# Kernel tuning notes

Measured on AMD Instinct MI355X. Metric: run time of the kernel, lower is better.

Reference implementation:

```python
import jax, jax.numpy as jnp
import numpy as np

ALPHA = 0.2  # LeakyReLU negative slope


def setup_inputs() -> dict:
    key = jax.random.key(0)
    k1, k2, k3, k4 = jax.random.split(key, 4)
    N, E, d_in, d_out = 100000, 1600000, 64, 64
    node_features = jax.random.normal(k1, (N, d_in), dtype=jnp.float32)
    edge_index = jax.random.randint(k2, (2, E), 0, N, dtype=jnp.int64)
    # learned params: W is Linear(in,out,bias=False) weight used as x @ W.T; store as [d_in,d_out]
    W = jax.random.normal(k3, (d_in, d_out), dtype=jnp.float32) * (1.414 * np.sqrt(2.0 / (d_in + d_out)))
    a = jax.random.normal(k4, (2 * d_out,), dtype=jnp.float32) * (1.414 * np.sqrt(2.0 / (2 * d_out + 1)))
    return {"node_features": node_features, "edge_index": edge_index, "W": W, "a": a}


def reference(node_features, edge_index, W, a):
    N = node_features.shape[0]
    d_out = W.shape[1]
    src, tgt = edge_index[0], edge_index[1]

    h = node_features @ W  # [N, d_out]
    # a([h_src, h_tgt]) == h_src @ a[:d] + h_tgt @ a[d:]; compute node-level scores once
    s_src = h @ a[:d_out]   # [N]
    s_tgt = h @ a[d_out:]   # [N]
    e = jax.nn.leaky_relu(s_src[src] + s_tgt[tgt], negative_slope=ALPHA)  # [E]

    # per-target segment softmax (stable): scatter-max, exp, scatter-sum
    m = jax.ops.segment_max(e, tgt, num_segments=N)          # [N]
    e_exp = jnp.exp(e - m[tgt])                              # [E]
    denom = jax.ops.segment_sum(e_exp, tgt, num_segments=N)  # [N]
    attention = e_exp / denom[tgt]                           # [E]
    # dropout is identity in eval mode (training=False)

    # weighted scatter-add of source features into targets
    h_prime = jax.ops.segment_sum(h[src] * attention[:, None], tgt, num_segments=N)  # [N, d_out]
    return jax.nn.elu(h_prime)
```

## Files before the change

kernel.cpp:

```cpp
#include <hip/hip_runtime.h>
#include <hip/hip_bf16.h>
#include <math.h>

#define ALPHA  0.2f
#define BSH    7
#define BNODES 128
#define NBMAX  1024
#define K_CH   4096
#define CAPB   3584

static __device__ __forceinline__ unsigned short f2bf(float x) {
    __hip_bfloat16 b = __float2bfloat16(x);
    return *reinterpret_cast<unsigned short*>(&b);
}

__global__ __launch_bounds__(256) void k_prep(
    const float* __restrict__ X, const float* __restrict__ W,
    const float* __restrict__ a, unsigned short* __restrict__ hb,
    float* __restrict__ s_src, float* __restrict__ s_tgt,
    const int* __restrict__ src, const int* __restrict__ tgt,
    int* __restrict__ cur, int* __restrict__ ebuf,
    int N, int E, int nb, int nbA)
{
    __shared__ __align__(16) char smem[33792];
    const int tid = threadIdx.x;

    if (blockIdx.x < nbA) {
        float (*XsT)[68] = (float(*)[68])smem;
        float (*Ws)[64]  = (float(*)[64])(smem + 17408);
        const int row0 = blockIdx.x * 64;

        {
            const float4* W4 = (const float4*)W;
            float4* Wd = (float4*)&Ws[0][0];
            for (int q = tid; q < 1024; q += 256) Wd[q] = W4[q];
        }
        for (int q = tid; q < 1024; q += 256) {
            int r  = q >> 4;
            int c4 = (q & 15) * 4;
            int row = row0 + r;
            float4 v = make_float4(0.f, 0.f, 0.f, 0.f);
            if (row < N) v = *(const float4*)&X[(size_t)row * 64 + c4];
            XsT[c4 + 0][r] = v.x; XsT[c4 + 1][r] = v.y;
            XsT[c4 + 2][r] = v.z; XsT[c4 + 3][r] = v.w;
        }
        __syncthreads();

        const int cg = (tid & 15) * 4;
        const int rg = (tid >> 4) * 4;

        float acc[4][4];
#pragma unroll
        for (int r = 0; r < 4; ++r)
#pragma unroll
            for (int c = 0; c < 4; ++c) acc[r][c] = 0.f;

#pragma unroll 8
        for (int k = 0; k < 64; ++k) {
            float4 wv = *(const float4*)&Ws[k][cg];
            float4 xv = *(const float4*)&XsT[k][rg];
            acc[0][0] += xv.x * wv.x; acc[0][1] += xv.x * wv.y; acc[0][2] += xv.x * wv.z; acc[0][3] += xv.x * wv.w;
            acc[1][0] += xv.y * wv.x; acc[1][1] += xv.y * wv.y; acc[1][2] += xv.y * wv.z; acc[1][3] += xv.y * wv.w;
            acc[2][0] += xv.z * wv.x; acc[2][1] += xv.z * wv.y; acc[2][2] += xv.z * wv.z; acc[2][3] += xv.z * wv.w;
            acc[3][0] += xv.w * wv.x; acc[3][1] += xv.w * wv.y; acc[3][2] += xv.w * wv.z; acc[3][3] += xv.w * wv.w;
        }

        float a1[4], a2[4];
#pragma unroll
        for (int c = 0; c < 4; ++c) { a1[c] = a[cg + c]; a2[c] = a[64 + cg + c]; }

#pragma unroll
        for (int r = 0; r < 4; ++r) {
            int row = row0 + rg + r;
            if (row < N) {
                ushort4 hv;
                hv.x = f2bf(acc[r][0]); hv.y = f2bf(acc[r][1]);
                hv.z = f2bf(acc[r][2]); hv.w = f2bf(acc[r][3]);
                *(ushort4*)&hb[(size_t)row * 64 + cg] = hv;
            }
            float v1 = acc[r][0]*a1[0] + acc[r][1]*a1[1] + acc[r][2]*a1[2] + acc[r][3]*a1[3];
            float v2 = acc[r][0]*a2[0] + acc[r][1]*a2[1] + acc[r][2]*a2[2] + acc[r][3]*a2[3];
            v1 += __shfl_xor(v1, 1); v2 += __shfl_xor(v2, 1);
            v1 += __shfl_xor(v1, 2); v2 += __shfl_xor(v2, 2);
            v1 += __shfl_xor(v1, 4); v2 += __shfl_xor(v2, 4);
            v1 += __shfl_xor(v1, 8); v2 += __shfl_xor(v2, 8);
            if ((tid & 15) == 0 && row < N) { s_src[row] = v1; s_tgt[row] = v2; }
        }
    } else {
        int* pk    = (int*)smem;
        int* hist  = (int*)(smem + 16384);
        int* off_s = (int*)(smem + 20480);
        int* gbase = (int*)(smem + 24576);
        int* gcap  = (int*)(smem + 28672);

        const int blk = blockIdx.x - nbA;
        const int e0  = blk * K_CH;
        const int e1  = min(e0 + K_CH, E);
        const int cnt = e1 - e0;

        for (int i = tid; i < nb; i += 256) hist[i] = 0;
        __syncthreads();

        for (int i = e0 + tid; i < e1; i += 256)
            atomicAdd(&hist[tgt[i] >> BSH], 1);
        __syncthreads();

        if (tid < 64) {
            int carry = 0;
            for (int base = 0; base < nb; base += 64) {
                int i = base + tid;
                int v = (i < nb) ? hist[i] : 0;
                int incl = v;
#pragma unroll
                for (int o = 1; o < 64; o <<= 1) {
                    int t2 = __shfl_up(incl, o);
                    if (tid >= o) incl += t2;
                }
                if (i < nb) off_s[i] = carry + incl - v;
                carry += __shfl(incl, 63);
            }
        }
        __syncthreads();

        for (int i = tid; i < nb; i += 256) {
            int c = hist[i];
            if (c) {
                int within = atomicAdd(&cur[i], c);
                gbase[i] = i * CAPB + within;
                gcap[i]  = CAPB - within;
            }
            hist[i] = off_s[i];
        }
        __syncthreads();

        for (int i = e0 + tid; i < e1; i += 256) {
            int t = tgt[i];
            int b = t >> BSH;
            int p = atomicAdd(&hist[b], 1);
            pk[p] = src[i] | ((t & (BNODES - 1)) << 17);
        }
        __syncthreads();

        for (int i = tid; i < cnt; i += 256) {
            int lo = 0, hi = nb;
            while (hi - lo > 1) {
                int mid = (lo + hi) >> 1;
                if (off_s[mid] <= i) lo = mid; else hi = mid;
            }
            int rel = i - off_s[lo];
            if (rel < gcap[lo]) ebuf[gbase[lo] + rel] = pk[i];
        }
    }
}

__global__ __launch_bounds__(512) void k_bgather(
    const int* __restrict__ cur, const int* __restrict__ ebuf,
    const float* __restrict__ s_src, const float* __restrict__ s_tgt,
    const uint2* __restrict__ hb2,
    float* __restrict__ out, int N)
{
    __shared__ int   ssrc[CAPB];
    __shared__ float sexp[CAPB];
    __shared__ int   hist[BNODES];
    __shared__ int   off_s[BNODES + 1];
    __shared__ int   cur_s[BNODES];
    __shared__ float sT[BNODES];

    const int tid  = threadIdx.x;
    const int b    = blockIdx.x;
    const int base = b << BSH;
    const int nn   = min(BNODES, N - base);
    const int beg  = b * CAPB;
    const int cnt  = min(cur[b], CAPB);

    if (tid < BNODES) {
        hist[tid] = 0;
        sT[tid] = (base + tid < N) ? s_tgt[base + tid] : 0.f;
    }
    __syncthreads();

    for (int i = tid; i < cnt; i += 512)
        atomicAdd(&hist[(ebuf[beg + i] >> 17) & (BNODES - 1)], 1);
    __syncthreads();

    if (tid < 64) {
        int carry = 0;
#pragma unroll
        for (int cb = 0; cb < BNODES; cb += 64) {
            int i = cb + tid;
            int v = hist[i];
            int incl = v;
#pragma unroll
            for (int o = 1; o < 64; o <<= 1) {
                int t2 = __shfl_up(incl, o);
                if (tid >= o) incl += t2;
            }
            off_s[i + 1] = carry + incl;
            cur_s[i]     = carry + incl - v;
            carry += __shfl(incl, 63);
        }
        if (tid == 0) off_s[0] = 0;
    }
    __syncthreads();

    for (int i = tid; i < cnt; i += 512) {
        int pkv  = ebuf[beg + i];
        int toff = (pkv >> 17) & (BNODES - 1);
        int sv   = pkv & 0x1FFFF;
        int pos  = atomicAdd(&cur_s[toff], 1);
        float sc = s_src[sv] + sT[toff];
        sc = (sc >= 0.f) ? sc : ALPHA * sc;
        ssrc[pos] = sv;
        sexp[pos] = __expf(sc);
    }
    __syncthreads();

    const int w     = tid >> 6;
    const int lane  = tid & 63;
    const int g     = lane >> 4;
    const int fidx2 = lane & 15;

    for (int tl = w; tl < nn; tl += 8) {
        const int t    = base + tl;
        const int beg2 = off_s[tl];
        const int c    = off_s[tl + 1] - beg2;
        const unsigned ocol = (unsigned)t * 64 + fidx2 * 4;

        if (c == 0) {
            if (g == 0) *(float4*)&out[ocol] = make_float4(0.f, 0.f, 0.f, 0.f);
            continue;
        }

        float ax = 0.f, ay = 0.f, az = 0.f, aw = 0.f, den = 0.f;
        for (int k = 0; k < c; k += 4) {
            int idx = k + g;
            int cl  = beg2 + min(idx, c - 1);
            int sv  = ssrc[cl];
            float pe = (idx < c) ? sexp[cl] : 0.f;
            uint2 u = hb2[((unsigned)sv << 4) + fidx2];
            den += pe;
            ax += pe * __uint_as_float(u.x << 16);
            ay += pe * __uint_as_float(u.x & 0xFFFF0000u);
            az += pe * __uint_as_float(u.y << 16);
            aw += pe * __uint_as_float(u.y & 0xFFFF0000u);
        }
        ax += __shfl_xor(ax, 16); ay += __shfl_xor(ay, 16);
        az += __shfl_xor(az, 16); aw += __shfl_xor(aw, 16);
        den += __shfl_xor(den, 16);
        ax += __shfl_xor(ax, 32); ay += __shfl_xor(ay, 32);
        az += __shfl_xor(az, 32); aw += __shfl_xor(aw, 32);
        den += __shfl_xor(den, 32);

        if (g == 0) {
            float rd = 1.f / den;
            float r0 = ax * rd, r1 = ay * rd, r2 = az * rd, r3 = aw * rd;
            r0 = (r0 > 0.f) ? r0 : expm1f(r0);
            r1 = (r1 > 0.f) ? r1 : expm1f(r1);
            r2 = (r2 > 0.f) ? r2 : expm1f(r2);
            r3 = (r3 > 0.f) ? r3 : expm1f(r3);
            *(float4*)&out[ocol] = make_float4(r0, r1, r2, r3);
        }
    }
}

extern "C" void kernel_launch(void* const* d_in, const int* in_sizes, int n_in,
                              void* d_out, int out_size, void* d_ws, size_t ws_size,
                              hipStream_t stream)
{
    const float* X  = (const float*)d_in[0];
    const int*   ei = (const int*)d_in[1];
    const float* W  = (const float*)d_in[2];
    const float* a  = (const float*)d_in[3];

    const int N = in_sizes[0] / 64;
    const int E = in_sizes[1] / 2;
    const int* src = ei;
    const int* tgt = ei + E;

    float* out = (float*)d_out;

    const int nb    = (N + BNODES - 1) >> BSH;
    const int nbA   = (N + 63) / 64;
    const int gFill = (E + K_CH - 1) / K_CH;

    char* ws = (char*)d_ws;
    unsigned short* hb = (unsigned short*)ws; ws += (size_t)N * 64 * sizeof(unsigned short);
    float* s_src  = (float*)ws; ws += (size_t)N * sizeof(float);
    float* s_tgt  = (float*)ws; ws += (size_t)N * sizeof(float);
    int*   cur    = (int*)ws;   ws += (size_t)nb * sizeof(int);
    int*   ebuf   = (int*)ws;   ws += (size_t)nb * CAPB * sizeof(int);

    hipMemsetAsync(cur, 0, (size_t)nb * sizeof(int), stream);

    k_prep    <<<nbA + gFill, 256, 0, stream>>>(X, W, a, hb, s_src, s_tgt,
                                                src, tgt, cur, ebuf, N, E, nb, nbA);
    k_bgather <<<nb, 512, 0, stream>>>(cur, ebuf, s_src, s_tgt,
                                       (const uint2*)hb, out, N);
}
```

Measured before the change: 120.4 us.

## Halve target bucket size to 64 nodes and shrink gather blocks to 256 threads

Targets are now bucketed 64 nodes at a time instead of 128, so there are about 1563 buckets with capacity 2048 each. Each gather block runs 256 threads with a single-wave scan, and its smaller LDS footprint allows more resident blocks and finer load balance across CUs. The per-bucket capacity check now comes from the bucket base offset rather than a separate array. The prep GEMM switches from a transposed X tile to a row-major tile with padding of 65, trading float4 X loads for scalar loads. Risks include more atomics on the global bucket counters and less headroom per bucket, since edges past capacity are silently dropped.

```diff
diff --git a/kernel.cpp b/kernel.cpp
--- a/kernel.cpp
+++ b/kernel.cpp
@@ -3,11 +3,11 @@
 #include <math.h>
 
 #define ALPHA  0.2f
-#define BSH    7
-#define BNODES 128
-#define NBMAX  1024
+#define BSH    6
+#define BNODES 64
+#define NBMAX  1600
 #define K_CH   4096
-#define CAPB   3584
+#define CAPB   2048
 
 static __device__ __forceinline__ unsigned short f2bf(float x) {
     __hip_bfloat16 b = __float2bfloat16(x);
@@ -22,12 +22,12 @@
     int* __restrict__ cur, int* __restrict__ ebuf,
     int N, int E, int nb, int nbA)
 {
-    __shared__ __align__(16) char smem[33792];
+    __shared__ __align__(16) char smem[35584];
     const int tid = threadIdx.x;
 
     if (blockIdx.x < nbA) {
-        float (*XsT)[68] = (float(*)[68])smem;
-        float (*Ws)[64]  = (float(*)[64])(smem + 17408);
+        float (*Xs)[65] = (float(*)[65])smem;
+        float (*Ws)[64] = (float(*)[64])(smem + 16640);
         const int row0 = blockIdx.x * 64;
 
         {
@@ -41,8 +41,8 @@
             int row = row0 + r;
             float4 v = make_float4(0.f, 0.f, 0.f, 0.f);
             if (row < N) v = *(const float4*)&X[(size_t)row * 64 + c4];
-            XsT[c4 + 0][r] = v.x; XsT[c4 + 1][r] = v.y;
-            XsT[c4 + 2][r] = v.z; XsT[c4 + 3][r] = v.w;
+            Xs[r][c4 + 0] = v.x; Xs[r][c4 + 1] = v.y;
+            Xs[r][c4 + 2] = v.z; Xs[r][c4 + 3] = v.w;
         }
         __syncthreads();
 
@@ -58,11 +58,12 @@
 #pragma unroll 8
         for (int k = 0; k < 64; ++k) {
             float4 wv = *(const float4*)&Ws[k][cg];
-            float4 xv = *(const float4*)&XsT[k][rg];
-            acc[0][0] += xv.x * wv.x; acc[0][1] += xv.x * wv.y; acc[0][2] += xv.x * wv.z; acc[0][3] += xv.x * wv.w;
-            acc[1][0] += xv.y * wv.x; acc[1][1] += xv.y * wv.y; acc[1][2] += xv.y * wv.z; acc[1][3] += xv.y * wv.w;
-            acc[2][0] += xv.z * wv.x; acc[2][1] += xv.z * wv.y; acc[2][2] += xv.z * wv.z; acc[2][3] += xv.z * wv.w;
-            acc[3][0] += xv.w * wv.x; acc[3][1] += xv.w * wv.y; acc[3][2] += xv.w * wv.z; acc[3][3] += xv.w * wv.w;
+            float x0 = Xs[rg + 0][k], x1 = Xs[rg + 1][k];
+            float x2 = Xs[rg + 2][k], x3 = Xs[rg + 3][k];
+            acc[0][0] += x0 * wv.x; acc[0][1] += x0 * wv.y; acc[0][2] += x0 * wv.z; acc[0][3] += x0 * wv.w;
+            acc[1][0] += x1 * wv.x; acc[1][1] += x1 * wv.y; acc[1][2] += x1 * wv.z; acc[1][3] += x1 * wv.w;
+            acc[2][0] += x2 * wv.x; acc[2][1] += x2 * wv.y; acc[2][2] += x2 * wv.z; acc[2][3] += x2 * wv.w;
+            acc[3][0] += x3 * wv.x; acc[3][1] += x3 * wv.y; acc[3][2] += x3 * wv.z; acc[3][3] += x3 * wv.w;
         }
 
         float a1[4], a2[4];
@@ -89,9 +90,8 @@
     } else {
         int* pk    = (int*)smem;
         int* hist  = (int*)(smem + 16384);
-        int* off_s = (int*)(smem + 20480);
-        int* gbase = (int*)(smem + 24576);
-        int* gcap  = (int*)(smem + 28672);
+        int* off_s = (int*)(smem + 22784);
+        int* gbase = (int*)(smem + 29184);
 
         const int blk = blockIdx.x - nbA;
         const int e0  = blk * K_CH;
@@ -127,7 +127,6 @@
             if (c) {
                 int within = atomicAdd(&cur[i], c);
                 gbase[i] = i * CAPB + within;
-                gcap[i]  = CAPB - within;
             }
             hist[i] = off_s[i];
         }
@@ -148,12 +147,13 @@
                 if (off_s[mid] <= i) lo = mid; else hi = mid;
             }
             int rel = i - off_s[lo];
-            if (rel < gcap[lo]) ebuf[gbase[lo] + rel] = pk[i];
-        }
-    }
-}
-
-__global__ __launch_bounds__(512) void k_bgather(
+            int gb  = gbase[lo];
+            if ((gb & (CAPB - 1)) + rel < CAPB) ebuf[gb + rel] = pk[i];
+        }
+    }
+}
+
+__global__ __launch_bounds__(256) void k_bgather(
     const int* __restrict__ cur, const int* __restrict__ ebuf,
     const float* __restrict__ s_src, const float* __restrict__ s_tgt,
     const uint2* __restrict__ hb2,
@@ -179,31 +179,25 @@
     }
     __syncthreads();
 
-    for (int i = tid; i < cnt; i += 512)
+    for (int i = tid; i < cnt; i += 256)
         atomicAdd(&hist[(ebuf[beg + i] >> 17) & (BNODES - 1)], 1);
     __syncthreads();
 
     if (tid < 64) {
-        int carry = 0;
-#pragma unroll
-        for (int cb = 0; cb < BNODES; cb += 64) {
-            int i = cb + tid;
-            int v = hist[i];
-            int incl = v;
-#pragma unroll
-            for (int o = 1; o < 64; o <<= 1) {
-                int t2 = __shfl_up(incl, o);
-                if (tid >= o) incl += t2;
-            }
-            off_s[i + 1] = carry + incl;
-            cur_s[i]     = carry + incl - v;
-            carry += __shfl(incl, 63);
-        }
+        int v = hist[tid];
+        int incl = v;
+#pragma unroll
+        for (int o = 1; o < 64; o <<= 1) {
+            int t2 = __shfl_up(incl, o);
+            if (tid >= o) incl += t2;
+        }
+        off_s[tid + 1] = incl;
+        cur_s[tid]     = incl - v;
         if (tid == 0) off_s[0] = 0;
     }
     __syncthreads();
 
-    for (int i = tid; i < cnt; i += 512) {
+    for (int i = tid; i < cnt; i += 256) {
         int pkv  = ebuf[beg + i];
         int toff = (pkv >> 17) & (BNODES - 1);
         int sv   = pkv & 0x1FFFF;
@@ -220,7 +214,7 @@
     const int g     = lane >> 4;
     const int fidx2 = lane & 15;
 
-    for (int tl = w; tl < nn; tl += 8) {
+    for (int tl = w; tl < nn; tl += 4) {
         const int t    = base + tl;
         const int beg2 = off_s[tl];
         const int c    = off_s[tl + 1] - beg2;
@@ -294,6 +288,6 @@
 
     k_prep    <<<nbA + gFill, 256, 0, stream>>>(X, W, a, hb, s_src, s_tgt,
                                                 src, tgt, cur, ebuf, N, E, nb, nbA);
-    k_bgather <<<nb, 512, 0, stream>>>(cur, ebuf, s_src, s_tgt,
+    k_bgather <<<nb, 256, 0, stream>>>(cur, ebuf, s_src, s_tgt,
                                        (const uint2*)hb, out, N);
 }
```

After: 124.4 us. +3.3%, slower.
